# Kernel tuning notes

Measured on AMD Instinct MI355X. Metric: run time of the kernel, lower is better.

## Reference

```python
import jax, jax.numpy as jnp
import numpy as np

HID = 2048
HEADS = 16
HEAD = HID // HEADS  # 128
INTER = 8192
EPS = 1e-5
THETA = 10000.0
B, S = 2, 2048


def _layernorm(x, scale, bias):
    mu = jnp.mean(x, axis=-1, keepdims=True)
    var = jnp.var(x, axis=-1, keepdims=True)
    return (x - mu) * jax.lax.rsqrt(var + EPS) * scale + bias


def _rope(x, cos, sin):
    # x: [b,s,h,d]; adjacent pairs form complex numbers (per apply_rotary_emb)
    xr = x.reshape(*x.shape[:-1], HEAD // 2, 2)
    x0, x1 = xr[..., 0], xr[..., 1]
    o0 = x0 * cos - x1 * sin
    o1 = x0 * sin + x1 * cos
    return jnp.stack((o0, o1), axis=-1).reshape(x.shape)


def setup_inputs() -> dict:
    key = jax.random.key(0)
    ks = jax.random.split(key, 6)
    sc = 0.02
    return {
        "hidden_states": jax.random.normal(ks[0], (B, S, HID), jnp.float32),
        "attention_mask": jnp.zeros((B, 1, 1, S), jnp.float32),
        "w_qkv": (jax.random.normal(ks[1], (HID, 3 * HID), jnp.float32) * sc),
        "b_qkv": jnp.zeros((3 * HID,), jnp.float32),
        "w_o": (jax.random.normal(ks[2], (HID, HID), jnp.float32) * sc),
        "b_o": jnp.zeros((HID,), jnp.float32),
        "ln1_scale": jnp.ones((HID,), jnp.float32),
        "ln1_bias": jnp.zeros((HID,), jnp.float32),
        "ln2_scale": jnp.ones((HID,), jnp.float32),
        "ln2_bias": jnp.zeros((HID,), jnp.float32),
        "w_in": (jax.random.normal(ks[3], (HID, INTER), jnp.float32) * sc),
        "b_in": jnp.zeros((INTER,), jnp.float32),
        "w_out": (jax.random.normal(ks[4], (INTER, HID), jnp.float32) * sc),
        "b_out": jnp.zeros((HID,), jnp.float32),
    }


def reference(hidden_states, attention_mask, w_qkv, b_qkv, w_o, b_o,
              ln1_scale, ln1_bias, ln2_scale, ln2_bias,
              w_in, b_in, w_out, b_out):
    b, s, d = hidden_states.shape
    # ---- attention branch ----
    x1 = _layernorm(hidden_states, ln1_scale, ln1_bias)
    qkv = x1 @ w_qkv + b_qkv
    q, k, v = jnp.split(qkv, 3, axis=-1)
    q = q.reshape(b, s, HEADS, HEAD)
    k = k.reshape(b, s, HEADS, HEAD)
    v = v.reshape(b, s, HEADS, HEAD)
    # rotary embedding (complex pairing of adjacent elements)
    inv_freq = 1.0 / (THETA ** (jnp.arange(0, HEAD, 2, dtype=jnp.float32) / HEAD))
    freqs = jnp.arange(s, dtype=jnp.float32)[:, None] * inv_freq[None, :]  # [s, HEAD/2]
    cos = jnp.cos(freqs)[None, :, None, :]
    sin = jnp.sin(freqs)[None, :, None, :]
    q = _rope(q, cos, sin)
    k = _rope(k, cos, sin)
    # NOTE: source multiplies by sqrt(head_size) (faithful to original code)
    factor = jnp.sqrt(jnp.float32(HEAD))
    attn = jnp.einsum('bqhd,bkhd->bhqk', q, k) * factor  # [b,h,s,s]
    causal = jnp.tril(jnp.ones((s, s), dtype=bool))
    bias = jnp.where(causal, 0.0, jnp.finfo(jnp.float32).min)
    attn = attn + bias[None, None, :, :] + attention_mask
    p = jax.nn.softmax(attn, axis=-1)
    ao = jnp.einsum('bhqk,bkhd->bqhd', p, v).reshape(b, s, d)
    attn_out = ao @ w_o + b_o
    # ---- mlp branch (parallel residual) ----
    x2 = _layernorm(hidden_states, ln2_scale, ln2_bias)
    mlp = jax.nn.gelu(x2 @ w_in + b_in, approximate=False) @ w_out + b_out
    return mlp + hidden_states + attn_out
```

## Files before the change

### kernel.cpp

```cpp
#include <hip/hip_runtime.h>
#include <math.h>

#define HID 2048
#define NH 16
#define HD 128
#define INTER 8192
#define BB 2
#define SS 2048
#define MT (BB*SS)

typedef __bf16 bf16x8 __attribute__((ext_vector_type(8)));
typedef _Float16 f16x8 __attribute__((ext_vector_type(8)));
typedef float f32x4 __attribute__((ext_vector_type(4)));
typedef unsigned short u16x8 __attribute__((ext_vector_type(8)));

__device__ __forceinline__ float bf2f(unsigned short u) {
  unsigned v = ((unsigned)u) << 16;
  return __builtin_bit_cast(float, v);
}
__device__ __forceinline__ unsigned short f2bf(float x) {
  unsigned u = __builtin_bit_cast(unsigned, x);
  u += 0x7fffu + ((u >> 16) & 1u);
  return (unsigned short)(u >> 16);
}
__device__ __forceinline__ unsigned short f2h(float x) {
  _Float16 h = (_Float16)x;
  return __builtin_bit_cast(unsigned short, h);
}
__device__ __forceinline__ void gll16(const void* g, const void* lds) {
  __builtin_amdgcn_global_load_lds(
      (const __attribute__((address_space(1))) void*)g,
      (__attribute__((address_space(3))) void*)lds, 16, 0, 0);
}

__global__ __launch_bounds__(256) void ln2k(
    const float* __restrict__ X, const float* __restrict__ s1,
    const float* __restrict__ b1, const float* __restrict__ s2,
    const float* __restrict__ b2, unsigned short* __restrict__ X1f,
    unsigned short* __restrict__ X2) {
  const int row = blockIdx.x;
  const int tid = threadIdx.x;
  const float* x = X + (long)row * HID;
  float4 v0 = ((const float4*)x)[tid * 2];
  float4 v1 = ((const float4*)x)[tid * 2 + 1];
  float s = v0.x + v0.y + v0.z + v0.w + v1.x + v1.y + v1.z + v1.w;
  float q = v0.x * v0.x + v0.y * v0.y + v0.z * v0.z + v0.w * v0.w +
            v1.x * v1.x + v1.y * v1.y + v1.z * v1.z + v1.w * v1.w;
#pragma unroll
  for (int off = 1; off < 64; off <<= 1) {
    s += __shfl_xor(s, off);
    q += __shfl_xor(q, off);
  }
  __shared__ float rs[4], rq[4];
  const int wid = tid >> 6, lane = tid & 63;
  if (lane == 0) { rs[wid] = s; rq[wid] = q; }
  __syncthreads();
  s = rs[0] + rs[1] + rs[2] + rs[3];
  q = rq[0] + rq[1] + rq[2] + rq[3];
  const float mu = s * (1.f / HID);
  const float var = q * (1.f / HID) - mu * mu;
  const float rstd = rsqrtf(var + 1e-5f);
  float xv[8] = {v0.x, v0.y, v0.z, v0.w, v1.x, v1.y, v1.z, v1.w};
  u16x8 o1, o2;
#pragma unroll
  for (int e = 0; e < 8; e++) {
    const int j = tid * 8 + e;
    const float xn = (xv[e] - mu) * rstd;
    o1[e] = f2h(xn * s1[j] + b1[j]);
    o2[e] = f2bf(xn * s2[j] + b2[j]);
  }
  *(u16x8*)(X1f + (long)row * HID + tid * 8) = o1;
  *(u16x8*)(X2 + (long)row * HID + tid * 8) = o2;
}

template <bool F16>
__global__ __launch_bounds__(256) void wtrans(const float* __restrict__ W,
                                              unsigned short* __restrict__ WT,
                                              int K, int N, int ldn, int coff) {
  (void)N;
  __shared__ float t[32][33];
  const int n0 = blockIdx.x * 32, k0 = blockIdx.y * 32;
  const int tx = threadIdx.x, ty = threadIdx.y;
#pragma unroll
  for (int r = 0; r < 4; r++)
    t[ty + r * 8][tx] = W[(long)(k0 + ty + r * 8) * ldn + coff + n0 + tx];
  __syncthreads();
#pragma unroll
  for (int r = 0; r < 4; r++) {
    const float v = t[tx][ty + r * 8];
    WT[(long)(n0 + ty + r * 8) * K + k0 + tx] = F16 ? f2h(v) : f2bf(v);
  }
}

__global__ void rope_tab(float2* __restrict__ rope) {
  const int s = blockIdx.x, i = threadIdx.x;
  const double ang = (double)s * pow(10000.0, -(double)i / 64.0);
  rope[s * 64 + i] = make_float2((float)cos(ang), (float)sin(ang));
}

__global__ __launch_bounds__(256) void gemmqkv(
    const unsigned short* __restrict__ A, const unsigned short* __restrict__ Bt,
    const float* __restrict__ bias, const float2* __restrict__ rope,
    unsigned short* __restrict__ QF, unsigned short* __restrict__ KF,
    unsigned short* __restrict__ Vb) {
  __shared__ unsigned short As[128 * 64];
  __shared__ unsigned short Bs[128 * 64];
  const int K = HID;
  const int tid = threadIdx.x;
  const int wid = tid >> 6, lane = tid & 63;
  const int l16 = lane & 15, lhi = lane >> 4;
  const int bn = blockIdx.x, bm = blockIdx.y;
  const int wr = wid >> 1, wc = wid & 1;
  const long rA0 = (long)bm * 128;
  const long rB0 = (long)bn * 128;

  f32x4 acc[4][4] = {};

  for (int kt = 0; kt < K; kt += 64) {
#pragma unroll
    for (int i = 0; i < 4; i++) {
      const int lin = i * 4096 + wid * 1024 + (lane << 4);
      const int row = lin >> 7;
      const int cs = ((lin >> 4) & 7) ^ (row & 7);
      gll16(A + (rA0 + row) * (long)K + kt + cs * 8,
            (const char*)As + (i * 4096 + wid * 1024));
      gll16(Bt + (rB0 + row) * (long)K + kt + cs * 8,
            (const char*)Bs + (i * 4096 + wid * 1024));
    }
    __syncthreads();
#pragma unroll
    for (int ks = 0; ks < 2; ks++) {
      f16x8 av[4], bv[4];
#pragma unroll
      for (int m = 0; m < 4; m++) {
        const int row = wr * 64 + m * 16 + l16;
        const int ch = (ks * 4 + lhi) ^ (row & 7);
        av[m] = *(const f16x8*)((const char*)As + row * 128 + ch * 16);
      }
#pragma unroll
      for (int n = 0; n < 4; n++) {
        const int row = wc * 64 + n * 16 + l16;
        const int ch = (ks * 4 + lhi) ^ (row & 7);
        bv[n] = *(const f16x8*)((const char*)Bs + row * 128 + ch * 16);
      }
#pragma unroll
      for (int m = 0; m < 4; m++)
#pragma unroll
        for (int n = 0; n < 4; n++)
          acc[m][n] = __builtin_amdgcn_mfma_f32_16x16x32_f16(av[m], bv[n],
                                                             acc[m][n], 0, 0, 0);
    }
    __syncthreads();
  }

  const int b_ = (int)(rA0 >> 11);
#pragma unroll
  for (int m = 0; m < 4; m++) {
#pragma unroll
    for (int n = 0; n < 4; n++) {
      const int col = (int)rB0 + wc * 64 + n * 16 + l16;
      const float bsv = bias[col];
      const int cq = col & 2047;
      const int i = (cq & 127) >> 1;
      const int hh = (cq >> 7) & 15;
      const int d = cq & 127;
#pragma unroll
      for (int r = 0; r < 4; r++) {
        const int row = (int)rA0 + wr * 64 + m * 16 + lhi * 4 + r;
        const int srow = row & 2047;
        const float v = acc[m][n][r] + bsv;
        if (col < 4096) {
          const float p = __shfl_xor(v, 1);
          const float2 cs = rope[srow * 64 + i];
          const float o = ((lane & 1) == 0) ? (v * cs.x - p * cs.y)
                                            : (p * cs.y + v * cs.x);
          unsigned short* dst = (col < 2048) ? QF : KF;
          dst[((long)(b_ * NH + hh) * SS + srow) * HD + d] = f2h(o);
        } else {
          Vb[(long)row * HID + (col - 4096)] = f2bf(v);
        }
      }
    }
  }
}

__global__ __launch_bounds__(256) void vtrans(
    const unsigned short* __restrict__ Vb, unsigned short* __restrict__ VTb) {
  __shared__ unsigned short t[32][33];
  const int bh = blockIdx.z, b = bh >> 4, h = bh & 15;
  const int d0 = blockIdx.x * 32, s0 = blockIdx.y * 32;
  const int tx = threadIdx.x, ty = threadIdx.y;
#pragma unroll
  for (int r = 0; r < 4; r++) {
    const int s = s0 + ty + r * 8;
    t[ty + r * 8][tx] = Vb[((long)(b * SS + s)) * HID + h * HD + d0 + tx];
  }
  __syncthreads();
#pragma unroll
  for (int r = 0; r < 4; r++) {
    const int d = d0 + ty + r * 8;
    VTb[((long)bh * HD + d) * SS + s0 + tx] = t[tx][ty + r * 8];
  }
}

template <int MODE>
__global__ __launch_bounds__(256) void gemm128(
    const unsigned short* __restrict__ A, const unsigned short* __restrict__ Bt,
    const float* __restrict__ bias, void* __restrict__ Cout, int M, int N,
    int K, const float* __restrict__ residF,
    const unsigned short* __restrict__ residB) {
  (void)M;
  __shared__ unsigned short As[128 * 64];
  __shared__ unsigned short Bs[128 * 64];
  const int tid = threadIdx.x;
  const int wid = tid >> 6, lane = tid & 63;
  const int l16 = lane & 15, lhi = lane >> 4;
  const int bn = blockIdx.x, bm = blockIdx.y;
  const int wr = wid >> 1, wc = wid & 1;
  const long rA0 = (long)bm * 128;
  const long rB0 = (long)bn * 128;

  f32x4 acc[4][4] = {};

  for (int kt = 0; kt < K; kt += 64) {
#pragma unroll
    for (int i = 0; i < 4; i++) {
      const int lin = i * 4096 + wid * 1024 + (lane << 4);
      const int row = lin >> 7;
      const int cs = ((lin >> 4) & 7) ^ (row & 7);
      gll16(A + (rA0 + row) * (long)K + kt + cs * 8,
            (const char*)As + (i * 4096 + wid * 1024));
      gll16(Bt + (rB0 + row) * (long)K + kt + cs * 8,
            (const char*)Bs + (i * 4096 + wid * 1024));
    }
    __syncthreads();
#pragma unroll
    for (int ks = 0; ks < 2; ks++) {
      bf16x8 av[4], bv[4];
#pragma unroll
      for (int m = 0; m < 4; m++) {
        const int row = wr * 64 + m * 16 + l16;
        const int ch = (ks * 4 + lhi) ^ (row & 7);
        av[m] = *(const bf16x8*)((const char*)As + row * 128 + ch * 16);
      }
#pragma unroll
      for (int n = 0; n < 4; n++) {
        const int row = wc * 64 + n * 16 + l16;
        const int ch = (ks * 4 + lhi) ^ (row & 7);
        bv[n] = *(const bf16x8*)((const char*)Bs + row * 128 + ch * 16);
      }
#pragma unroll
      for (int m = 0; m < 4; m++)
#pragma unroll
        for (int n = 0; n < 4; n++)
          acc[m][n] = __builtin_amdgcn_mfma_f32_16x16x32_bf16(av[m], bv[n],
                                                              acc[m][n], 0, 0, 0);
    }
    __syncthreads();
  }

#pragma unroll
  for (int m = 0; m < 4; m++) {
#pragma unroll
    for (int n = 0; n < 4; n++) {
      const long col = rB0 + wc * 64 + n * 16 + l16;
      const float bsv = bias[col];
#pragma unroll
      for (int r = 0; r < 4; r++) {
        const long row = rA0 + wr * 64 + m * 16 + lhi * 4 + r;
        float v = acc[m][n][r] + bsv;
        if (MODE == 1) v = 0.5f * v * (1.f + erff(v * 0.7071067811865475f));
        if (MODE == 2) {
          v += residF[row * N + col] + bf2f(residB[row * N + col]);
          ((float*)Cout)[row * N + col] = v;
        } else {
          ((unsigned short*)Cout)[row * N + col] = f2bf(v);
        }
      }
    }
  }
}

__global__ __launch_bounds__(512, 2) void flash(
    const unsigned short* __restrict__ QF, const unsigned short* __restrict__ KF,
    const unsigned short* __restrict__ VT, const float* __restrict__ amask,
    unsigned short* __restrict__ AO) {
  __shared__ unsigned short Kt[2][64 * 128];
  __shared__ unsigned short Vt[2][128 * 64];
  __shared__ unsigned short Pl[8 * 1024];
  __shared__ float maskL[SS];
  const int z = blockIdx.x;
  const int qt = 15 - (z >> 5);
  const int bh = z & 31;
  const int b = bh >> 4, h = bh & 15;
  const int tid = threadIdx.x, wid = tid >> 6, lane = tid & 63;
  const int l16 = lane & 15, lhi = lane >> 4;
  const unsigned short* Qfb = QF + (long)bh * SS * HD;
  const unsigned short* Kfb = KF + (long)bh * SS * HD;
  const unsigned short* Vb = VT + (long)bh * HD * SS;
  const int q0 = qt * 128 + wid * 16;
  const float LOG2E = 1.4426950408889634f;
  const float SCL2 = 16.322232154552f;

  {
    float4 m0 = ((const float4*)(amask + (long)b * SS))[tid];
    m0.x *= LOG2E; m0.y *= LOG2E; m0.z *= LOG2E; m0.w *= LOG2E;
    ((float4*)maskL)[tid] = m0;
  }

  f16x8 qf[4];
#pragma unroll
  for (int ks = 0; ks < 4; ks++)
    qf[ks] = *(const f16x8*)(Qfb + (long)(q0 + l16) * HD + ks * 32 + lhi * 8);

  auto stage = [&](int kt2, int bu) {
#pragma unroll
    for (int i = 0; i < 2; i++) {
      const int lin = i * 8192 + wid * 1024 + (lane << 4);
      const int dst = i * 8192 + wid * 1024;
      {
        const int row = lin >> 8;
        const int cs = ((lin >> 4) & 15) ^ (row & 7);
        gll16(Kfb + (long)(kt2 * 64 + row) * HD + cs * 8,
              (const char*)Kt[bu] + dst);
      }
      {
        const int row = lin >> 7;
        const int cs = ((lin >> 4) & 7) ^ (row & 7);
        gll16(Vb + (long)row * SS + kt2 * 64 + cs * 8, (const char*)Vt[bu] + dst);
      }
    }
  };

  f32x4 accO[8] = {};
  float mrow[4], lrow[4];
#pragma unroll
  for (int r = 0; r < 4; r++) { mrow[r] = -3e38f; lrow[r] = 0.f; }

  const int nkt = 2 * qt + 2;
  stage(0, 0);
  asm volatile("s_waitcnt lgkmcnt(0)" ::: "memory");
  int buf = 0;
  for (int kt = 0; kt < nkt; kt++) {
    if (kt + 1 < nkt) {
      stage(kt + 1, buf ^ 1);
      asm volatile("s_waitcnt vmcnt(4)" ::: "memory");
    } else {
      asm volatile("s_waitcnt vmcnt(0)" ::: "memory");
    }
    __builtin_amdgcn_s_barrier();

    const bool active = (kt * 64 <= q0 + 15);
    if (active) {
      f32x4 accS[4] = {};
      __builtin_amdgcn_s_setprio(1);
#pragma unroll
      for (int ks = 0; ks < 4; ks++) {
        f16x8 bk[4];
#pragma unroll
        for (int nf = 0; nf < 4; nf++) {
          const int row = nf * 16 + l16;
          const int ch = (ks * 4 + lhi) ^ (row & 7);
          bk[nf] = *(const f16x8*)((const char*)Kt[buf] + row * 256 + ch * 16);
        }
#pragma unroll
        for (int nf = 0; nf < 4; nf++)
          accS[nf] = __builtin_amdgcn_mfma_f32_16x16x32_f16(qf[ks], bk[nf],
                                                            accS[nf], 0, 0, 0);
      }
      __builtin_amdgcn_s_setprio(0);

      float mk[4];
#pragma unroll
      for (int nf = 0; nf < 4; nf++) mk[nf] = maskL[kt * 64 + nf * 16 + l16];
#pragma unroll
      for (int nf = 0; nf < 4; nf++)
#pragma unroll
        for (int r = 0; r < 4; r++) {
          const int key = kt * 64 + nf * 16 + l16;
          const int qg = q0 + lhi * 4 + r;
          const float sv = accS[nf][r] * SCL2 + mk[nf];
          accS[nf][r] = (key > qg) ? -1e30f : sv;
        }

      float mx[4];
#pragma unroll
      for (int r = 0; r < 4; r++) {
        float m0 = fmaxf(fmaxf(accS[0][r], accS[1][r]),
                         fmaxf(accS[2][r], accS[3][r]));
        m0 = fmaxf(m0, __shfl_xor(m0, 1));
        m0 = fmaxf(m0, __shfl_xor(m0, 2));
        m0 = fmaxf(m0, __shfl_xor(m0, 4));
        m0 = fmaxf(m0, __shfl_xor(m0, 8));
        mx[r] = m0;
      }
      bool defer = true;
#pragma unroll
      for (int r = 0; r < 4; r++) defer = defer && (mx[r] <= mrow[r] + 8.f);
      if (!__all(defer)) {
#pragma unroll
        for (int r = 0; r < 4; r++) {
          const float mnew = fmaxf(mrow[r], mx[r]);
          const float alpha = exp2f(mrow[r] - mnew);
          mrow[r] = mnew;
          lrow[r] *= alpha;
#pragma unroll
          for (int nf2 = 0; nf2 < 8; nf2++) accO[nf2][r] *= alpha;
        }
      }
#pragma unroll
      for (int r = 0; r < 4; r++) {
        const int rowl = lhi * 4 + r;
        const int qg = q0 + rowl;
        float rsum = 0.f;
#pragma unroll
        for (int nf = 0; nf < 4; nf++) {
          const int key = kt * 64 + nf * 16 + l16;
          const float p = (key > qg) ? 0.f : exp2f(accS[nf][r] - mrow[r]);
          rsum += p;
          const int colv = nf * 16 + l16;
          const int slot = (colv >> 3) ^ (rowl & 7);
          *(unsigned short*)((char*)Pl + wid * 2048 + rowl * 128 + slot * 16 +
                             (colv & 7) * 2) = f2bf(p);
        }
        rsum += __shfl_xor(rsum, 1);
        rsum += __shfl_xor(rsum, 2);
        rsum += __shfl_xor(rsum, 4);
        rsum += __shfl_xor(rsum, 8);
        lrow[r] += rsum;
      }

      __builtin_amdgcn_s_setprio(1);
#pragma unroll
      for (int ks2 = 0; ks2 < 2; ks2++) {
        const int chp = (ks2 * 4 + lhi) ^ (l16 & 7);
        bf16x8 pa =
            *(const bf16x8*)((const char*)Pl + wid * 2048 + l16 * 128 + chp * 16);
#pragma unroll
        for (int nf2 = 0; nf2 < 8; nf2++) {
          const int rowv = nf2 * 16 + l16;
          const int ch = (ks2 * 4 + lhi) ^ (rowv & 7);
          bf16x8 vv =
              *(const bf16x8*)((const char*)Vt[buf] + rowv * 128 + ch * 16);
          accO[nf2] = __builtin_amdgcn_mfma_f32_16x16x32_bf16(pa, vv,
                                                              accO[nf2], 0, 0, 0);
        }
      }
      __builtin_amdgcn_s_setprio(0);
    }
    __builtin_amdgcn_s_barrier();
    buf ^= 1;
  }

#pragma unroll
  for (int nf2 = 0; nf2 < 8; nf2++)
#pragma unroll
    for (int r = 0; r < 4; r++) {
      const int qg = q0 + lhi * 4 + r;
      const int d = nf2 * 16 + l16;
      const float v = accO[nf2][r] / lrow[r];
      AO[((long)(b * SS + qg)) * HID + h * HD + d] = f2bf(v);
    }
}

extern "C" void kernel_launch(void* const* d_in, const int* in_sizes, int n_in,
                              void* d_out, int out_size, void* d_ws,
                              size_t ws_size, hipStream_t stream) {
  (void)in_sizes; (void)n_in; (void)out_size;
  const float* hidden = (const float*)d_in[0];
  const float* amask = (const float*)d_in[1];
  const float* w_qkv = (const float*)d_in[2];
  const float* b_qkv = (const float*)d_in[3];
  const float* w_o = (const float*)d_in[4];
  const float* b_o = (const float*)d_in[5];
  const float* ln1s = (const float*)d_in[6];
  const float* ln1b = (const float*)d_in[7];
  const float* ln2s = (const float*)d_in[8];
  const float* ln2b = (const float*)d_in[9];
  const float* w_in = (const float*)d_in[10];
  const float* b_in = (const float*)d_in[11];
  const float* w_out = (const float*)d_in[12];
  const float* b_out = (const float*)d_in[13];

  char* ws = (char*)d_ws;
  unsigned short* X1f = (unsigned short*)(ws + 0);
  unsigned short* X2  = (unsigned short*)(ws + 16777216);
  unsigned short* Vbf = (unsigned short*)(ws + 33554432);
  unsigned short* WQ  = (unsigned short*)(ws + 50331648);
  unsigned short* QFb = (unsigned short*)(ws + 75497472);
  unsigned short* KFb = (unsigned short*)(ws + 92274688);
  unsigned short* VTb = (unsigned short*)(ws + 109051904);
  unsigned short* ATT = (unsigned short*)(ws + 125829120);
  unsigned short* WD  = (unsigned short*)(ws + 142606336);
  float2* ROPE = (float2*)(ws + 176160768);
  if (ws_size < 177209344) return;

  unsigned short* AO = X1f;
  unsigned short* H1 = WQ;

  ln2k<<<MT, 256, 0, stream>>>(hidden, ln1s, ln1b, ln2s, ln2b, X1f, X2);
  rope_tab<<<SS, 64, 0, stream>>>(ROPE);
  wtrans<true><<<dim3(192, 64), dim3(32, 8), 0, stream>>>(w_qkv, WQ, HID,
                                                          3 * HID, 3 * HID, 0);
  gemmqkv<<<dim3(48, 32), 256, 0, stream>>>(X1f, WQ, b_qkv, ROPE, QFb, KFb,
                                            Vbf);
  vtrans<<<dim3(4, 64, 32), dim3(32, 8), 0, stream>>>(Vbf, VTb);
  flash<<<512, 512, 0, stream>>>(QFb, KFb, VTb, amask, AO);
  wtrans<false><<<dim3(64, 64), dim3(32, 8), 0, stream>>>(w_o, WD, HID, HID,
                                                          HID, 0);
  gemm128<0><<<dim3(16, 32), 256, 0, stream>>>(AO, WD, b_o, ATT, MT, HID, HID,
                                               nullptr, nullptr);
  wtrans<false><<<dim3(256, 64), dim3(32, 8), 0, stream>>>(w_in, WD, HID,
                                                           INTER, INTER, 0);
  gemm128<1><<<dim3(64, 32), 256, 0, stream>>>(X2, WD, b_in, H1, MT, INTER,
                                               HID, nullptr, nullptr);
  wtrans<false><<<dim3(64, 256), dim3(32, 8), 0, stream>>>(w_out, WD, INTER,
                                                           HID, HID, 0);
  gemm128<2><<<dim3(16, 32), 256, 0, stream>>>(H1, WD, b_out, d_out, MT, HID,
                                               INTER, hidden, ATT);
}
```

Before: 756.2 us.

## Use 256x256 double-buffered GEMM tiles with split-K for MLP down-projection

Replaces the 128x128 QKV and MLP up-projection GEMMs with a templated 256x256-tile, 512-thread kernel. It double-buffers LDS loads with explicit vmcnt waits and raises wave priority around the MFMA section. The MLP down-projection becomes a 2-way split-K writing fp32 partials, followed by a separate elementwise kernel that adds the partials, bias, residual and attention output. The goal is more data reuse per tile and overlap of global loads with compute. The cost is larger LDS use, higher register pressure, fewer blocks on the wide-N GEMMs, and extra fp32 partial traffic plus one more launch.

```diff
diff --git a/kernel.cpp b/kernel.cpp
--- a/kernel.cpp
+++ b/kernel.cpp
@@ -98,90 +98,140 @@
   rope[s * 64 + i] = make_float2((float)cos(ang), (float)sin(ang));
 }
 
-__global__ __launch_bounds__(256) void gemmqkv(
+template <int MODE, bool F16>
+__global__ __launch_bounds__(512, 2) void gemm256(
     const unsigned short* __restrict__ A, const unsigned short* __restrict__ Bt,
-    const float* __restrict__ bias, const float2* __restrict__ rope,
-    unsigned short* __restrict__ QF, unsigned short* __restrict__ KF,
-    unsigned short* __restrict__ Vb) {
-  __shared__ unsigned short As[128 * 64];
-  __shared__ unsigned short Bs[128 * 64];
-  const int K = HID;
+    const float* __restrict__ bias, void* __restrict__ Cout, int N, int K,
+    const float2* __restrict__ rope, unsigned short* __restrict__ QF,
+    unsigned short* __restrict__ KF, unsigned short* __restrict__ Vb,
+    float* __restrict__ P1) {
+  __shared__ unsigned short As[2][256 * 64];
+  __shared__ unsigned short Bs[2][256 * 64];
   const int tid = threadIdx.x;
   const int wid = tid >> 6, lane = tid & 63;
   const int l16 = lane & 15, lhi = lane >> 4;
-  const int bn = blockIdx.x, bm = blockIdx.y;
-  const int wr = wid >> 1, wc = wid & 1;
-  const long rA0 = (long)bm * 128;
-  const long rB0 = (long)bn * 128;
-
-  f32x4 acc[4][4] = {};
-
-  for (int kt = 0; kt < K; kt += 64) {
+  const int wr = wid >> 2, wc = wid & 3;
+  const long rA0 = (long)blockIdx.y * 256;
+  const long rB0 = (long)blockIdx.x * 256;
+  const int nkt = (MODE == 4) ? (K / 128) : (K / 64);
+  const int k0 = (MODE == 4) ? (int)blockIdx.z * (K / 2) : 0;
+
+  f32x4 acc[8][4] = {};
+
+  auto stage = [&](int kt2, int bu) {
 #pragma unroll
     for (int i = 0; i < 4; i++) {
-      const int lin = i * 4096 + wid * 1024 + (lane << 4);
+      const int lin = i * 8192 + tid * 16;
       const int row = lin >> 7;
       const int cs = ((lin >> 4) & 7) ^ (row & 7);
-      gll16(A + (rA0 + row) * (long)K + kt + cs * 8,
-            (const char*)As + (i * 4096 + wid * 1024));
-      gll16(Bt + (rB0 + row) * (long)K + kt + cs * 8,
-            (const char*)Bs + (i * 4096 + wid * 1024));
-    }
-    __syncthreads();
+      const int dst = i * 8192 + wid * 1024;
+      const long g = k0 + kt2 * 64 + cs * 8;
+      gll16(A + (rA0 + row) * (long)K + g, (const char*)As[bu] + dst);
+      gll16(Bt + (rB0 + row) * (long)K + g, (const char*)Bs[bu] + dst);
+    }
+  };
+
+  stage(0, 0);
+  int buf = 0;
+  for (int kt = 0; kt < nkt; kt++) {
+    if (kt + 1 < nkt) {
+      stage(kt + 1, buf ^ 1);
+      asm volatile("s_waitcnt vmcnt(8)" ::: "memory");
+    } else {
+      asm volatile("s_waitcnt vmcnt(0)" ::: "memory");
+    }
+    __builtin_amdgcn_s_barrier();
+
+    __builtin_amdgcn_s_setprio(1);
 #pragma unroll
     for (int ks = 0; ks < 2; ks++) {
-      f16x8 av[4], bv[4];
-#pragma unroll
-      for (int m = 0; m < 4; m++) {
-        const int row = wr * 64 + m * 16 + l16;
-        const int ch = (ks * 4 + lhi) ^ (row & 7);
-        av[m] = *(const f16x8*)((const char*)As + row * 128 + ch * 16);
-      }
+      u16x8 bv[4], av[8];
 #pragma unroll
       for (int n = 0; n < 4; n++) {
         const int row = wc * 64 + n * 16 + l16;
         const int ch = (ks * 4 + lhi) ^ (row & 7);
-        bv[n] = *(const f16x8*)((const char*)Bs + row * 128 + ch * 16);
-      }
-#pragma unroll
-      for (int m = 0; m < 4; m++)
-#pragma unroll
-        for (int n = 0; n < 4; n++)
-          acc[m][n] = __builtin_amdgcn_mfma_f32_16x16x32_f16(av[m], bv[n],
-                                                             acc[m][n], 0, 0, 0);
-    }
-    __syncthreads();
+        bv[n] = *(const u16x8*)((const char*)Bs[buf] + row * 128 + ch * 16);
+      }
+#pragma unroll
+      for (int m = 0; m < 8; m++) {
+        const int row = wr * 128 + m * 16 + l16;
+        const int ch = (ks * 4 + lhi) ^ (row & 7);
+        av[m] = *(const u16x8*)((const char*)As[buf] + row * 128 + ch * 16);
+      }
+#pragma unroll
+      for (int m = 0; m < 8; m++)
+#pragma unroll
+        for (int n = 0; n < 4; n++) {
+          if constexpr (F16)
+            acc[m][n] = __builtin_amdgcn_mfma_f32_16x16x32_f16(
+                __builtin_bit_cast(f16x8, av[m]),
+                __builtin_bit_cast(f16x8, bv[n]), acc[m][n], 0, 0, 0);
+          else
+            acc[m][n] = __builtin_amdgcn_mfma_f32_16x16x32_bf16(
+                __builtin_bit_cast(bf16x8, av[m]),
+                __builtin_bit_cast(bf16x8, bv[n]), acc[m][n], 0, 0, 0);
+        }
+    }
+    __builtin_amdgcn_s_setprio(0);
+    __builtin_amdgcn_s_barrier();
+    buf ^= 1;
   }
 
   const int b_ = (int)(rA0 >> 11);
 #pragma unroll
-  for (int m = 0; m < 4; m++) {
+  for (int m = 0; m < 8; m++) {
 #pragma unroll
     for (int n = 0; n < 4; n++) {
       const int col = (int)rB0 + wc * 64 + n * 16 + l16;
-      const float bsv = bias[col];
+      const float bsv = (MODE == 4) ? 0.f : bias[col];
       const int cq = col & 2047;
       const int i = (cq & 127) >> 1;
       const int hh = (cq >> 7) & 15;
       const int d = cq & 127;
 #pragma unroll
       for (int r = 0; r < 4; r++) {
-        const int row = (int)rA0 + wr * 64 + m * 16 + lhi * 4 + r;
-        const int srow = row & 2047;
-        const float v = acc[m][n][r] + bsv;
-        if (col < 4096) {
-          const float p = __shfl_xor(v, 1);
-          const float2 cs = rope[srow * 64 + i];
-          const float o = ((lane & 1) == 0) ? (v * cs.x - p * cs.y)
-                                            : (p * cs.y + v * cs.x);
-          unsigned short* dst = (col < 2048) ? QF : KF;
-          dst[((long)(b_ * NH + hh) * SS + srow) * HD + d] = f2h(o);
-        } else {
-          Vb[(long)row * HID + (col - 4096)] = f2bf(v);
-        }
-      }
-    }
-  }
+        const long row = rA0 + wr * 128 + m * 16 + lhi * 4 + r;
+        float v = acc[m][n][r] + bsv;
+        if (MODE == 1) {
+          v = 0.5f * v * (1.f + erff(v * 0.7071067811865475f));
+          ((unsigned short*)Cout)[row * N + col] = f2bf(v);
+        } else if (MODE == 4) {
+          float* dst = blockIdx.z ? P1 : (float*)Cout;
+          dst[row * N + col] = v;
+        } else if (MODE == 3) {
+          const int srow = (int)row & 2047;
+          if (col < 4096) {
+            const float p = __shfl_xor(v, 1);
+            const float2 cs = rope[srow * 64 + i];
+            const float o = ((lane & 1) == 0) ? (v * cs.x - p * cs.y)
+                                              : (p * cs.y + v * cs.x);
+            unsigned short* dst = (col < 2048) ? QF : KF;
+            dst[((long)(b_ * NH + hh) * SS + srow) * HD + d] = f2h(o);
+          } else {
+            Vb[row * HID + (col - 4096)] = f2bf(v);
+          }
+        }
+      }
+    }
+  }
+}
+
+__global__ __launch_bounds__(256) void mlpfin(
+    const float* __restrict__ P0, const float* __restrict__ P1,
+    const float* __restrict__ bias, const float* __restrict__ hidden,
+    const unsigned short* __restrict__ ATT, float* __restrict__ out) {
+  const long i = ((long)blockIdx.x * 256 + threadIdx.x) * 4;
+  float4 a = *(const float4*)(P0 + i);
+  float4 b = *(const float4*)(P1 + i);
+  float4 hc = *(const float4*)(hidden + i);
+  ushort4 t = *(const ushort4*)(ATT + i);
+  float4 bs = *(const float4*)(bias + (int)(i & 2047));
+  float4 o;
+  o.x = a.x + b.x + bs.x + hc.x + bf2f(t.x);
+  o.y = a.y + b.y + bs.y + hc.y + bf2f(t.y);
+  o.z = a.z + b.z + bs.z + hc.z + bf2f(t.z);
+  o.w = a.w + b.w + bs.w + hc.w + bf2f(t.w);
+  *(float4*)(out + i) = o;
 }
 
 __global__ __launch_bounds__(256) void vtrans(
@@ -493,17 +543,19 @@
   unsigned short* ATT = (unsigned short*)(ws + 125829120);
   unsigned short* WD  = (unsigned short*)(ws + 142606336);
   float2* ROPE = (float2*)(ws + 176160768);
-  if (ws_size < 177209344) return;
+  float* P1 = (float*)(ws + 177209344);
+  if (ws_size < 210763776) return;
 
   unsigned short* AO = X1f;
   unsigned short* H1 = WQ;
+  float* P0 = (float*)ws;
 
   ln2k<<<MT, 256, 0, stream>>>(hidden, ln1s, ln1b, ln2s, ln2b, X1f, X2);
   rope_tab<<<SS, 64, 0, stream>>>(ROPE);
   wtrans<true><<<dim3(192, 64), dim3(32, 8), 0, stream>>>(w_qkv, WQ, HID,
                                                           3 * HID, 3 * HID, 0);
-  gemmqkv<<<dim3(48, 32), 256, 0, stream>>>(X1f, WQ, b_qkv, ROPE, QFb, KFb,
-                                            Vbf);
+  gemm256<3, true><<<dim3(24, 16), 512, 0, stream>>>(
+      X1f, WQ, b_qkv, nullptr, 3 * HID, HID, ROPE, QFb, KFb, Vbf, nullptr);
   vtrans<<<dim3(4, 64, 32), dim3(32, 8), 0, stream>>>(Vbf, VTb);
   flash<<<512, 512, 0, stream>>>(QFb, KFb, VTb, amask, AO);
   wtrans<false><<<dim3(64, 64), dim3(32, 8), 0, stream>>>(w_o, WD, HID, HID,
@@ -512,10 +564,11 @@
                                                nullptr, nullptr);
   wtrans<false><<<dim3(256, 64), dim3(32, 8), 0, stream>>>(w_in, WD, HID,
                                                            INTER, INTER, 0);
-  gemm128<1><<<dim3(64, 32), 256, 0, stream>>>(X2, WD, b_in, H1, MT, INTER,
-                                               HID, nullptr, nullptr);
+  gemm256<1, false><<<dim3(32, 16), 512, 0, stream>>>(
+      X2, WD, b_in, H1, INTER, HID, nullptr, nullptr, nullptr, nullptr, nullptr);
   wtrans<false><<<dim3(64, 256), dim3(32, 8), 0, stream>>>(w_out, WD, INTER,
                                                            HID, HID, 0);
-  gemm128<2><<<dim3(16, 32), 256, 0, stream>>>(H1, WD, b_out, d_out, MT, HID,
-                                               INTER, hidden, ATT);
-}
+  gemm256<4, false><<<dim3(8, 16, 2), 512, 0, stream>>>(
+      H1, WD, nullptr, P0, HID, INTER, nullptr, nullptr, nullptr, nullptr, P1);
+  mlpfin<<<8192, 256, 0, stream>>>(P0, P1, b_out, hidden, ATT, (float*)d_out);
+}
```

Measured after the change: 766.3 us. Within noise of the previous version (+1.3%).
